# Optimization experiments

Measured on AMD Instinct MI355X. Metric: run time of the kernel, lower is better.

Reference implementation:

```python
import jax, jax.numpy as jnp
import numpy as np
from jax import lax
import math

B, CH, BINS, CROP = 8, 2, 1024, 1024
NUM_BANDS = 4
FF = 2048
EPS = 1e-5
SCALE = 0.02  # weight init scale for numeric stability


def _inorm(x, g, b):
    # InstanceNorm2d: x [B, C, H, W], normalize over (H, W) per (B, C); biased var
    m = x.mean(axis=(2, 3), keepdims=True)
    v = x.var(axis=(2, 3), keepdims=True)
    return (x - m) / jnp.sqrt(v + EPS) * g[None, :, None, None] + b[None, :, None, None]


def _dwconv(x, k):
    # depthwise conv1d: x [B, bins, W], k [bins, 1, 3], padding=1, groups=bins
    return lax.conv_general_dilated(x, k, (1,), [(1, 1)],
                                    dimension_numbers=('NCH', 'OIH', 'NCH'),
                                    feature_group_count=x.shape[1])


def setup_inputs() -> dict:
    key = jax.random.key(0)
    ks = jax.random.split(key, 12)
    inp = {
        'x': jax.random.normal(ks[0], (B, CH, BINS, CROP), jnp.float32),
        'prev_qk': jax.random.normal(ks[1], (B, NUM_BANDS, CROP, CROP), jnp.float32),
        'g_in': jnp.ones((CROP,), jnp.float32),
        'b_in': jnp.zeros((CROP,), jnp.float32),
        'W_in': jax.random.normal(ks[2], (1, CH), jnp.float32) * SCALE,
        'bias_in': jnp.zeros((1,), jnp.float32),
        'g1': jnp.ones((CROP,), jnp.float32),
        'b1': jnp.zeros((CROP,), jnp.float32),
        'Wq': jax.random.normal(ks[3], (BINS, BINS), jnp.float32) * SCALE,
        'Wk': jax.random.normal(ks[4], (BINS, BINS), jnp.float32) * SCALE,
        'Wv': jax.random.normal(ks[5], (BINS, BINS), jnp.float32) * SCALE,
        'Wo': jax.random.normal(ks[6], (BINS, BINS), jnp.float32) * SCALE,
        'kq': jax.random.normal(ks[7], (BINS, 1, 3), jnp.float32) * SCALE,
        'kk': jax.random.normal(ks[8], (BINS, 1, 3), jnp.float32) * SCALE,
        'kv': jax.random.normal(ks[9], (BINS, 1, 3), jnp.float32) * SCALE,
        'pos_w': jax.random.normal(ks[10], (BINS // NUM_BANDS, CROP), jnp.float32) * SCALE,
        'g2': jnp.ones((CROP,), jnp.float32),
        'b2': jnp.zeros((CROP,), jnp.float32),
        'W_ff': jax.random.normal(ks[11], (1, 2), jnp.float32) * SCALE,
        'bias_ff': jnp.zeros((1,), jnp.float32),
        'W1': jax.random.normal(jax.random.fold_in(key, 100), (FF, BINS), jnp.float32) * SCALE,
        'W2': jax.random.normal(jax.random.fold_in(key, 101), (BINS, FF), jnp.float32) * SCALE,
    }
    return inp


def reference(x, prev_qk, g_in, b_in, W_in, bias_in, g1, b1, Wq, Wk, Wv, Wo,
              kq, kk, kv, pos_w, g2, b2, W_ff, bias_ff, W1, W2):
    b = x.shape[0]
    nb = NUM_BANDS
    hd = BINS // nb
    # in_norm + in_project: transposed layout [B, CROP, BINS, CH]
    xt = jnp.transpose(x, (0, 3, 2, 1))
    xt = _inorm(xt, g_in, b_in)
    xt = jnp.einsum('bwhc,oc->bwho', xt, W_in) + bias_in  # [B,CROP,BINS,1]
    x0 = jnp.transpose(xt, (0, 3, 2, 1))                  # [B,1,BINS,CROP]
    # norm1 + attention over frames (w == CROP, c == BINS)
    h = jnp.transpose(_inorm(jnp.transpose(x0, (0, 3, 2, 1)), g1, b1), (0, 3, 2, 1))
    a_in = jnp.transpose(h, (0, 3, 2, 1))[..., 0]         # [B, W, BINS]
    q = jnp.einsum('bwc,oc->bwo', a_in, Wq)
    q = jnp.transpose(_dwconv(jnp.transpose(q, (0, 2, 1)), kq), (0, 2, 1))
    k = jnp.einsum('bwc,oc->bwo', a_in, Wk)
    k = jnp.transpose(_dwconv(jnp.transpose(k, (0, 2, 1)), kk), (0, 2, 1))
    v = jnp.einsum('bwc,oc->bwo', a_in, Wv)
    v = jnp.transpose(_dwconv(jnp.transpose(v, (0, 2, 1)), kv), (0, 2, 1))
    q4 = jnp.transpose(q.reshape(b, CROP, nb, hd), (0, 2, 1, 3))   # [B,nb,W,hd]
    k4 = jnp.transpose(k.reshape(b, CROP, nb, hd), (0, 2, 3, 1))   # [B,nb,hd,W]
    v4 = jnp.transpose(v.reshape(b, CROP, nb, hd), (0, 2, 1, 3))   # [B,nb,W,hd]
    # relative-position bias via pad-and-shift
    p = jnp.matmul(q4, pos_w)                                      # [B,nb,W,CROP]
    p = jnp.pad(p, ((0, 0), (0, 0), (0, 0), (1, 0)))
    p = jnp.swapaxes(p, 2, 3)[:, :, 1:, :]                         # [B,nb,CROP,W]
    qk = (jnp.matmul(q4, k4) + p) / math.sqrt(BINS)
    qk = qk + prev_qk
    a = jax.nn.softmax(qk, axis=-1)
    o = jnp.transpose(jnp.matmul(a, v4), (0, 2, 1, 3)).reshape(b, CROP, BINS)
    o = jnp.einsum('bwc,oc->bwo', o, Wo)                           # [B,W,BINS]
    h4 = jnp.transpose(o[..., None], (0, 3, 2, 1))                 # [B,1,BINS,CROP]
    x1 = jnp.concatenate([x0, h4], axis=1)                         # [B,2,BINS,CROP]
    # norm2 + ff_project + squared-ReLU FFN
    hn = _inorm(jnp.transpose(x1, (0, 3, 2, 1)), g2, b2)           # [B,CROP,BINS,2]
    hn = jnp.einsum('bwhc,oc->bwho', hn, W_ff) + bias_ff           # [B,CROP,BINS,1]
    hn = jnp.transpose(hn, (0, 3, 2, 1))                           # [B,1,BINS,CROP]
    ht = jnp.swapaxes(hn, 2, 3)                                    # [B,1,CROP,BINS]
    ht = jnp.square(jax.nn.relu(jnp.einsum('bowc,fc->bowf', ht, W1)))
    ht = jnp.einsum('bowf,cf->bowc', ht, W2)
    hf = jnp.swapaxes(ht, 2, 3)                                    # [B,1,BINS,CROP]
    out = jnp.concatenate([x1, hf], axis=1)                        # [B,3,BINS,CROP]
    return out, qk
```

## Files before the change

kernel.cpp:

```cpp
#include <hip/hip_runtime.h>
#include <stdint.h>

#define DEVI __device__ __forceinline__

typedef __attribute__((ext_vector_type(8))) short bf16x8;
typedef __attribute__((ext_vector_type(4))) float f32x4;

#define B_    8
#define CROP_ 1024
#define BINS_ 1024
#define NB_   4
#define HD_   256
#define FF_   2048
#define EPSF  1e-5f
#define OUT0_ELEMS (8ull*3ull*1024ull*1024ull)
#define MBYTE (1024ull*1024ull)
#define M1ELEM (1024ll*1024ll)

DEVI unsigned short f2bf(float f) {
  unsigned u = __builtin_bit_cast(unsigned, f);
  u += 0x7fffu + ((u >> 16) & 1u);
  return (unsigned short)(u >> 16);
}
DEVI float bf2f(unsigned short h) {
  unsigned u = ((unsigned)h) << 16;
  return __builtin_bit_cast(float, u);
}

DEVI void gload16(const unsigned short* g, unsigned short* l) {
  __builtin_amdgcn_global_load_lds(
      (const __attribute__((address_space(1))) unsigned int*)g,
      (__attribute__((address_space(3))) unsigned int*)l, 16, 0, 0);
}

DEVI void stage32(const unsigned short* g, unsigned short* lds, int ld, int k0) {
  int t = threadIdx.x;
  int wv = t >> 6, ln = t & 63;
  int srow = wv*32 + (ln >> 2);
  int scol = (ln & 3)*8;
  const unsigned short* gp = g + (size_t)srow*ld + k0 + scol;
  gload16(gp, lds + wv*32*32);
  gload16(gp + (size_t)16*ld, lds + (wv*32 + 16)*32);
}

__global__ __launch_bounds__(256) void k_conv_all(
    const float* __restrict__ Wq, const float* __restrict__ Wk,
    const float* __restrict__ Wv, const float* __restrict__ Wo,
    const float* __restrict__ W1, const float* __restrict__ W2,
    const float* __restrict__ pw,
    unsigned short* __restrict__ WQKVB, unsigned short* __restrict__ WOB,
    unsigned short* __restrict__ W1B, unsigned short* __restrict__ W2B,
    unsigned short* __restrict__ PWT) {
  long long i = (long long)blockIdx.x*256 + threadIdx.x;
  long long stride = (long long)gridDim.x*256;
  const long long total = 8*M1ELEM + (1 << 18);
  for (; i < total; i += stride) {
    if (i < 3*M1ELEM) {
      const float* s = i < M1ELEM ? Wq : (i < 2*M1ELEM ? Wk : Wv);
      WQKVB[i] = f2bf(s[i & (M1ELEM-1)]);
    } else if (i < 4*M1ELEM) { WOB[i-3*M1ELEM] = f2bf(Wo[i-3*M1ELEM]); }
    else if (i < 6*M1ELEM)   { W1B[i-4*M1ELEM] = f2bf(W1[i-4*M1ELEM]); }
    else if (i < 8*M1ELEM)   { W2B[i-6*M1ELEM] = f2bf(W2[i-6*M1ELEM]); }
    else {
      long long j = i - 8*M1ELEM;
      int w = (int)(j >> 8), d = (int)(j & 255);
      PWT[j] = f2bf(pw[d*1024 + w]);
    }
  }
}

__global__ __launch_bounds__(256) void k_instat(const float* __restrict__ x,
                                                float* __restrict__ mean, float* __restrict__ rstd) {
  int b = blockIdx.y, w0 = blockIdx.x*32;
  int t = threadIdx.x, wl = t & 31, p = t >> 5;
  const float* xb = x + (size_t)b*2*BINS_*CROP_ + w0 + wl;
  float s = 0.f, ss = 0.f;
  for (int i = p*256; i < p*256 + 256; ++i) {
    float v = xb[(size_t)i*CROP_];
    s += v; ss += v*v;
  }
  __shared__ float ls[8][32], lss[8][32];
  ls[p][wl] = s; lss[p][wl] = ss;
  __syncthreads();
  if (t < 32) {
    float S = 0.f, SS = 0.f;
    for (int q = 0; q < 8; ++q) { S += ls[q][t]; SS += lss[q][t]; }
    float m = S*(1.f/2048.f);
    float var = SS*(1.f/2048.f) - m*m;
    mean[b*CROP_ + w0 + t] = m;
    rstd[b*CROP_ + w0 + t] = rsqrtf(var + EPSF);
  }
}

__global__ __launch_bounds__(256) void k_x0(const float* __restrict__ x,
    const float* __restrict__ mean, const float* __restrict__ rstd,
    const float* __restrict__ g_in, const float* __restrict__ b_in,
    const float* __restrict__ W_in, const float* __restrict__ bias_in,
    float* __restrict__ outp, float* __restrict__ x0t) {
  int b = blockIdx.z;
  int h0 = blockIdx.y*32, w0 = blockIdx.x*32;
  int tx = threadIdx.x, ty = threadIdx.y;
  float W0 = W_in[0], W1 = W_in[1], bi = bias_in[0];
  float sW = W0 + W1;
  __shared__ float tile[32][33];
  int w = w0 + tx;
  float m = mean[b*CROP_ + w], r = rstd[b*CROP_ + w];
  float coef = r * g_in[w];
  float add = b_in[w]*sW + bi;
  for (int s = 0; s < 4; ++s) {
    int h = h0 + ty + s*8;
    size_t i0 = (((size_t)b*2)*BINS_ + h)*CROP_ + w;
    float v0 = x[i0], v1 = x[i0 + (size_t)BINS_*CROP_];
    float val = coef*(W0*v0 + W1*v1 - m*sW) + add;
    outp[(((size_t)b*3)*BINS_ + h)*CROP_ + w] = val;
    tile[ty + s*8][tx] = val;
  }
  __syncthreads();
  for (int s = 0; s < 4; ++s) {
    int wl = ty + s*8;
    x0t[((size_t)b*CROP_ + w0 + wl)*BINS_ + h0 + tx] = tile[tx][wl];
  }
}

__global__ __launch_bounds__(256) void k_norm1(const float* __restrict__ x0t,
    const float* __restrict__ g1, const float* __restrict__ b1,
    unsigned short* __restrict__ ain) {
  int r = blockIdx.x;
  int w = r & (CROP_ - 1);
  int t = threadIdx.x;
  const float* row = x0t + (size_t)r*BINS_;
  float v[4], s = 0.f, ss = 0.f;
  for (int q = 0; q < 4; ++q) { v[q] = row[t + q*256]; s += v[q]; ss += v[q]*v[q]; }
  for (int off = 32; off; off >>= 1) { s += __shfl_xor(s, off); ss += __shfl_xor(ss, off); }
  __shared__ float red[8];
  int wv = t >> 6;
  if ((t & 63) == 0) { red[wv] = s; red[4 + wv] = ss; }
  __syncthreads();
  s = red[0] + red[1] + red[2] + red[3];
  ss = red[4] + red[5] + red[6] + red[7];
  float m = s*(1.f/1024.f);
  float var = ss*(1.f/1024.f) - m*m;
  float rs = rsqrtf(var + EPSF);
  float g = g1[w], bb = b1[w];
  for (int q = 0; q < 4; ++q)
    ain[(size_t)r*BINS_ + t + q*256] = f2bf((v[q] - m)*rs*g + bb);
}

__global__ __launch_bounds__(256) void k_norm2(const float* __restrict__ x0t,
    const float* __restrict__ o2,
    const float* __restrict__ g2, const float* __restrict__ b2,
    const float* __restrict__ W_ff, const float* __restrict__ bias_ff,
    unsigned short* __restrict__ hn) {
  int r = blockIdx.x;
  int w = r & (CROP_ - 1);
  int t = threadIdx.x;
  const float* ra = x0t + (size_t)r*BINS_;
  const float* rb = o2 + (size_t)r*BINS_;
  float va[4], vb[4], s = 0.f, ss = 0.f;
  for (int q = 0; q < 4; ++q) {
    va[q] = ra[t + q*256]; vb[q] = rb[t + q*256];
    s += va[q] + vb[q]; ss += va[q]*va[q] + vb[q]*vb[q];
  }
  for (int off = 32; off; off >>= 1) { s += __shfl_xor(s, off); ss += __shfl_xor(ss, off); }
  __shared__ float red[8];
  int wv = t >> 6;
  if ((t & 63) == 0) { red[wv] = s; red[4 + wv] = ss; }
  __syncthreads();
  s = red[0] + red[1] + red[2] + red[3];
  ss = red[4] + red[5] + red[6] + red[7];
  float m = s*(1.f/2048.f);
  float var = ss*(1.f/2048.f) - m*m;
  float rs = rsqrtf(var + EPSF);
  float W0 = W_ff[0], W1f = W_ff[1];
  float gg = g2[w]*rs;
  float add = b2[w]*(W0 + W1f) + bias_ff[0];
  for (int q = 0; q < 4; ++q)
    hn[(size_t)r*BINS_ + t + q*256] = f2bf(gg*(W0*(va[q] - m) + W1f*(vb[q] - m)) + add);
}

__global__ __launch_bounds__(256) void k_dwconv(const unsigned short* __restrict__ qkvb,
    const float* __restrict__ kq, const float* __restrict__ kk2, const float* __restrict__ kv,
    unsigned short* __restrict__ qkvc) {
  int w = blockIdx.x, b = blockIdx.y, which = blockIdx.z;
  int t = threadIdx.x;
  const float* kw = which == 0 ? kq : (which == 1 ? kk2 : kv);
  const unsigned short* r0 = qkvb + (size_t)which*8*M1ELEM + ((size_t)b*CROP_ + w)*BINS_;
  unsigned short* d0 = qkvc + (size_t)which*8*M1ELEM + ((size_t)b*CROP_ + w)*BINS_;
  for (int q = 0; q < 4; ++q) {
    int c = t + q*256;
    float k0 = kw[c*3], k1 = kw[c*3 + 1], k2 = kw[c*3 + 2];
    float acc = bf2f(r0[c]) * k1;
    if (w > 0)        acc += bf2f(r0[c - BINS_]) * k0;
    if (w < CROP_-1)  acc += bf2f(r0[c + BINS_]) * k2;
    d0[c] = f2bf(acc);
  }
}

__global__ __launch_bounds__(256) void k_tr_bf16(const unsigned short* __restrict__ src,
                                                 unsigned short* __restrict__ dst) {
  int b = blockIdx.z;
  int w0 = blockIdx.x*32, c0 = blockIdx.y*32;
  int tx = threadIdx.x, ty = threadIdx.y;
  __shared__ unsigned short tile[32][33];
  const unsigned short* S = src + (size_t)b*BINS_*CROP_;
  unsigned short* D = dst + (size_t)b*BINS_*CROP_;
  for (int s = 0; s < 4; ++s)
    tile[ty + s*8][tx] = S[(size_t)(w0 + ty + s*8)*BINS_ + c0 + tx];
  __syncthreads();
  for (int s = 0; s < 4; ++s)
    D[(size_t)(c0 + ty + s*8)*CROP_ + w0 + tx] = tile[tx][ty + s*8];
}

__global__ __launch_bounds__(256) void k_tr_f32_out(const float* __restrict__ src,
                                                    float* __restrict__ outp, int ch) {
  int b = blockIdx.z;
  int w0 = blockIdx.x*32, h0 = blockIdx.y*32;
  int tx = threadIdx.x, ty = threadIdx.y;
  __shared__ float tile[32][33];
  const float* S = src + (size_t)b*CROP_*BINS_;
  for (int s = 0; s < 4; ++s)
    tile[ty + s*8][tx] = S[(size_t)(w0 + ty + s*8)*BINS_ + h0 + tx];
  __syncthreads();
  float* D = outp + (((size_t)b*3 + ch)*BINS_)*CROP_;
  for (int s = 0; s < 4; ++s)
    D[(size_t)(h0 + ty + s*8)*CROP_ + w0 + tx] = tile[tx][ty + s*8];
}

#define BUFB 49152
#define ABYTES 32768

DEVI void stage_ab(const unsigned short* Ab, int lda, const unsigned short* Bb, int ldb,
                   int k0, unsigned short* buf, int t, int wv) {
  int trow = t >> 3;
  int colel = ((t & 7) ^ (trow & 7)) << 3;
  unsigned short* lbase = buf + wv*512;
  const unsigned short* ga = Ab + (size_t)trow*lda + k0 + colel;
#pragma unroll
  for (int c = 0; c < 4; ++c)
    gload16(ga + (size_t)(c*64)*lda, lbase + c*4096);
  const unsigned short* gb = Bb + (size_t)trow*ldb + k0 + colel;
  unsigned short* lbb = buf + 16384 + wv*512;
#pragma unroll
  for (int c = 0; c < 2; ++c)
    gload16(gb + (size_t)(c*64)*ldb, lbb + c*4096);
}

template<int MODE>
__global__ __launch_bounds__(512) void k_gemm3(
    const unsigned short* __restrict__ A, int lda,
    const unsigned short* __restrict__ Bt, int ldb,
    void* __restrict__ C, int ldc, int K)
{
  __shared__ __align__(16) unsigned short lds[3*24576];
  const unsigned short* Ab = A + (size_t)blockIdx.x*256*lda;
  const unsigned short* Bb = Bt + (size_t)blockIdx.y*128*ldb;
  const int t = threadIdx.x;
  const int wv = t >> 6, ln = t & 63;
  const int wm = wv >> 1, wn = wv & 1;
  const int lr = ln & 15, lk = ln >> 4;
  const int sx = (lr & 7) << 4;
  const int NT = K >> 6;
  stage_ab(Ab, lda, Bb, ldb, 0,   lds,           t, wv);
  stage_ab(Ab, lda, Bb, ldb, 64,  lds + 24576,   t, wv);
  stage_ab(Ab, lda, Bb, ldb, 128, lds + 49152,   t, wv);
  asm volatile("s_waitcnt vmcnt(12)" ::: "memory");
  __builtin_amdgcn_s_barrier();

  f32x4 acc[4][4] = {};
  for (int kt = 0; kt < NT; ++kt) {
    const int cur = kt % 3;
    const char* bufc = (const char*)lds + cur*BUFB;
    bf16x8 af[2][4], bf[2][4];
#pragma unroll
    for (int kk = 0; kk < 2; ++kk) {
#pragma unroll
      for (int mi = 0; mi < 4; ++mi) {
        int row = wm*64 + mi*16 + lr;
        af[kk][mi] = *(const bf16x8*)(bufc + ((row*128 + kk*64 + lk*16) ^ sx));
      }
#pragma unroll
      for (int ni = 0; ni < 4; ++ni) {
        int row = wn*64 + ni*16 + lr;
        bf[kk][ni] = *(const bf16x8*)(bufc + ABYTES + ((row*128 + kk*64 + lk*16) ^ sx));
      }
    }
    asm volatile("s_waitcnt lgkmcnt(0)" ::: "memory");
    __builtin_amdgcn_s_barrier();
    if (kt + 3 < NT)
      stage_ab(Ab, lda, Bb, ldb, (kt+3)*64, (unsigned short*)((char*)lds + cur*BUFB), t, wv);
    __builtin_amdgcn_s_setprio(1);
#pragma unroll
    for (int kk = 0; kk < 2; ++kk)
#pragma unroll
      for (int mi = 0; mi < 4; ++mi)
#pragma unroll
        for (int ni = 0; ni < 4; ++ni)
          acc[mi][ni] = __builtin_amdgcn_mfma_f32_16x16x32_bf16(af[kk][mi], bf[kk][ni], acc[mi][ni], 0, 0, 0);
    __builtin_amdgcn_s_setprio(0);
    if (kt + 1 < NT) {
      int rem = (NT-1 < kt+3 ? NT-1 : kt+3) - (kt+1);
      if (rem >= 2)      asm volatile("s_waitcnt vmcnt(12)" ::: "memory");
      else if (rem == 1) asm volatile("s_waitcnt vmcnt(6)"  ::: "memory");
      else               asm volatile("s_waitcnt vmcnt(0)"  ::: "memory");
      __builtin_amdgcn_s_barrier();
    }
  }

  const int row0 = blockIdx.x*256 + wm*64 + lk*4;
  const int col0 = blockIdx.y*128 + wn*64 + lr;
#pragma unroll
  for (int mi = 0; mi < 4; ++mi)
#pragma unroll
    for (int ni = 0; ni < 4; ++ni)
#pragma unroll
      for (int j = 0; j < 4; ++j) {
        int row = row0 + mi*16 + j;
        int col = col0 + ni*16;
        float v = acc[mi][ni][j];
        if (MODE == 0) {
          ((float*)C)[(size_t)row*ldc + col] = v;
        } else if (MODE == 2) {
          float rr = fmaxf(v, 0.f);
          ((unsigned short*)C)[(size_t)row*ldc + col] = f2bf(rr*rr);
        } else {
          ((unsigned short*)C)[(size_t)(col >> 10)*8*M1ELEM + (size_t)row*1024 + (col & 1023)] = f2bf(v);
        }
      }
}

__global__ __launch_bounds__(256) void k_qkpos(
    const unsigned short* __restrict__ qc, const unsigned short* __restrict__ kc,
    const unsigned short* __restrict__ pwt,
    const float* __restrict__ prev, float* __restrict__ qkout,
    float* __restrict__ Mg, float* __restrict__ Lg)
{
  __shared__ __align__(16) unsigned short lA1[128*32], lB1[128*32], lA2[128*32], lB2[128*32];
  const int z = blockIdx.z, b = z >> 2, n = z & 3;
  const size_t bandoff = (size_t)b*CROP_*BINS_ + (size_t)n*HD_;
  const unsigned short* A1 = qc + bandoff + (size_t)blockIdx.x*128*BINS_;
  const unsigned short* B1 = kc + bandoff + (size_t)blockIdx.y*128*BINS_;
  const unsigned short* A2 = pwt + (size_t)blockIdx.x*128*HD_;
  const unsigned short* B2 = qc + bandoff + (size_t)blockIdx.y*128*BINS_;
  const int t = threadIdx.x;
  const int wv = t >> 6, ln = t & 63;
  const int wr = (wv >> 1)*64, wc = (wv & 1)*64;
  const int lr = ln & 15, lk = ln >> 4;
  f32x4 acc[4][4] = {};
  for (int k0 = 0; k0 < HD_; k0 += 32) {
    stage32(A1, lA1, BINS_, k0);
    stage32(B1, lB1, BINS_, k0);
    stage32(A2, lA2, HD_, k0);
    stage32(B2, lB2, BINS_, k0);
    __syncthreads();
    bf16x8 af[4], bfr[4];
#pragma unroll
    for (int mi = 0; mi < 4; ++mi) af[mi]  = *(const bf16x8*)&lA1[(wr + mi*16 + lr)*32 + lk*8];
#pragma unroll
    for (int ni = 0; ni < 4; ++ni) bfr[ni] = *(const bf16x8*)&lB1[(wc + ni*16 + lr)*32 + lk*8];
#pragma unroll
    for (int mi = 0; mi < 4; ++mi)
#pragma unroll
      for (int ni = 0; ni < 4; ++ni)
        acc[mi][ni] = __builtin_amdgcn_mfma_f32_16x16x32_bf16(af[mi], bfr[ni], acc[mi][ni], 0, 0, 0);
#pragma unroll
    for (int mi = 0; mi < 4; ++mi) af[mi]  = *(const bf16x8*)&lA2[(wr + mi*16 + lr)*32 + lk*8];
#pragma unroll
    for (int ni = 0; ni < 4; ++ni) bfr[ni] = *(const bf16x8*)&lB2[(wc + ni*16 + lr)*32 + lk*8];
#pragma unroll
    for (int mi = 0; mi < 4; ++mi)
#pragma unroll
      for (int ni = 0; ni < 4; ++ni)
        acc[mi][ni] = __builtin_amdgcn_mfma_f32_16x16x32_bf16(af[mi], bfr[ni], acc[mi][ni], 0, 0, 0);
    __syncthreads();
  }
  const float* pz = prev + (size_t)z*CROP_*CROP_;
  float* oz = qkout + (size_t)z*CROP_*CROP_;
  const int row0 = blockIdx.x*128 + wr + lk*4;
  const int col0 = blockIdx.y*128 + wc + lr;
  float* smf = (float*)lA1;
  float* slf = smf + 256;
  const int wch = wv & 1;
  const int rbase = wr + lk*4;
#pragma unroll
  for (int mi = 0; mi < 4; ++mi) {
    float v[4][4];
    float tmax[4];
#pragma unroll
    for (int j = 0; j < 4; ++j) tmax[j] = -1e30f;
#pragma unroll
    for (int ni = 0; ni < 4; ++ni)
#pragma unroll
      for (int j = 0; j < 4; ++j) {
        size_t idx = (size_t)(row0 + mi*16 + j)*CROP_ + col0 + ni*16;
        float val = acc[mi][ni][j]*0.03125f + pz[idx];
        oz[idx] = val;
        v[j][ni] = val;
        tmax[j] = fmaxf(tmax[j], val);
      }
#pragma unroll
    for (int off = 1; off < 16; off <<= 1)
#pragma unroll
      for (int j = 0; j < 4; ++j) tmax[j] = fmaxf(tmax[j], __shfl_xor(tmax[j], off));
    if ((ln & 15) == 0)
#pragma unroll
      for (int j = 0; j < 4; ++j) smf[wch*128 + rbase + mi*16 + j] = tmax[j];
    __syncthreads();
    float mrow[4], psum[4];
#pragma unroll
    for (int j = 0; j < 4; ++j) {
      int rl = rbase + mi*16 + j;
      mrow[j] = fmaxf(smf[rl], smf[128 + rl]);
      psum[j] = 0.f;
#pragma unroll
      for (int ni = 0; ni < 4; ++ni) psum[j] += __expf(v[j][ni] - mrow[j]);
    }
#pragma unroll
    for (int off = 1; off < 16; off <<= 1)
#pragma unroll
      for (int j = 0; j < 4; ++j) psum[j] += __shfl_xor(psum[j], off);
    if ((ln & 15) == 0)
#pragma unroll
      for (int j = 0; j < 4; ++j) slf[wch*128 + rbase + mi*16 + j] = psum[j];
    __syncthreads();
    if (wch == 0 && (ln & 15) == 0) {
#pragma unroll
      for (int j = 0; j < 4; ++j) {
        int rl = rbase + mi*16 + j;
        int rg = blockIdx.x*128 + rl;
        size_t si = ((size_t)z*CROP_ + rg)*8 + blockIdx.y;
        Mg[si] = mrow[j];
        Lg[si] = slf[rl] + slf[128 + rl];
      }
    }
  }
}

__global__ __launch_bounds__(256) void k_pv(
    const float* __restrict__ qk, const float* __restrict__ Mg, const float* __restrict__ Lg,
    const unsigned short* __restrict__ vct, unsigned short* __restrict__ ob)
{
  __shared__ __align__(16) unsigned short lA[2*128*32];
  __shared__ __align__(16) unsigned short lB[2*128*32];
  __shared__ float s_m[128], s_il[128];
  const int z = blockIdx.z, b = z >> 2, band = z & 3;
  const int row0 = blockIdx.x*128;
  const int cy = blockIdx.y;
  const float* qkf = qk + (size_t)z*CROP_*CROP_ + (size_t)row0*CROP_;
  const unsigned short* Bb = vct + ((size_t)b*CROP_ + band*HD_ + cy*128)*CROP_;
  const int t = threadIdx.x;
  const int wv = t >> 6, ln = t & 63;
  const int wr = (wv >> 1)*64, wc = (wv & 1)*64;
  const int lr = ln & 15, lk = ln >> 4;
  if (t < 128) {
    size_t rg = (size_t)z*CROP_ + row0 + t;
    float m = -1e30f;
#pragma unroll
    for (int cb = 0; cb < 8; ++cb) m = fmaxf(m, Mg[rg*8 + cb]);
    float l = 0.f;
#pragma unroll
    for (int cb = 0; cb < 8; ++cb) l += Lg[rg*8 + cb]*__expf(Mg[rg*8 + cb] - m);
    s_m[t] = m;
    s_il[t] = 1.f / l;
  }
  __syncthreads();
  f32x4 acc[4][4] = {};
  for (int k0 = 0; k0 < CROP_; k0 += 64) {
#pragma unroll
    for (int chunk = 0; chunk < 2; ++chunk) {
#pragma unroll
      for (int i = 0; i < 4; ++i) {
        int idx = i*256 + t;
        int row = idx >> 3, f4 = idx & 7;
        const float4 vv = *(const float4*)&qkf[(size_t)row*CROP_ + k0 + chunk*32 + f4*4];
        float mr = s_m[row];
        unsigned lo = (unsigned)f2bf(__expf(vv.x - mr)) | ((unsigned)f2bf(__expf(vv.y - mr)) << 16);
        unsigned hi = (unsigned)f2bf(__expf(vv.z - mr)) | ((unsigned)f2bf(__expf(vv.w - mr)) << 16);
        *(uint2*)&lA[chunk*4096 + row*32 + f4*4] = make_uint2(lo, hi);
      }
    }
    stage32(Bb, lB, CROP_, k0);
    stage32(Bb, lB + 4096, CROP_, k0 + 32);
    __syncthreads();
#pragma unroll
    for (int kk = 0; kk < 2; ++kk) {
      bf16x8 af[4], bfr[4];
#pragma unroll
      for (int mi = 0; mi < 4; ++mi) af[mi]  = *(const bf16x8*)&lA[kk*4096 + (wr + mi*16 + lr)*32 + lk*8];
#pragma unroll
      for (int ni = 0; ni < 4; ++ni) bfr[ni] = *(const bf16x8*)&lB[kk*4096 + (wc + ni*16 + lr)*32 + lk*8];
#pragma unroll
      for (int mi = 0; mi < 4; ++mi)
#pragma unroll
        for (int ni = 0; ni < 4; ++ni)
          acc[mi][ni] = __builtin_amdgcn_mfma_f32_16x16x32_bf16(af[mi], bfr[ni], acc[mi][ni], 0, 0, 0);
    }
    __syncthreads();
  }
#pragma unroll
  for (int mi = 0; mi < 4; ++mi)
#pragma unroll
    for (int j = 0; j < 4; ++j) {
      int rl = wr + lk*4 + mi*16 + j;
      float il = s_il[rl];
#pragma unroll
      for (int ni = 0; ni < 4; ++ni) {
        int col = band*HD_ + cy*128 + wc + ni*16 + lr;
        ob[((size_t)b*CROP_ + row0 + rl)*BINS_ + col] = f2bf(acc[mi][ni][j]*il);
      }
    }
}

extern "C" void kernel_launch(void* const* d_in, const int* in_sizes, int n_in,
                              void* d_out, int out_size, void* d_ws, size_t ws_size,
                              hipStream_t stream) {
  (void)in_sizes; (void)n_in; (void)out_size; (void)ws_size;
  const float* x       = (const float*)d_in[0];
  const float* prev_qk = (const float*)d_in[1];
  const float* g_in    = (const float*)d_in[2];
  const float* b_in    = (const float*)d_in[3];
  const float* W_in    = (const float*)d_in[4];
  const float* bias_in = (const float*)d_in[5];
  const float* g1      = (const float*)d_in[6];
  const float* b1      = (const float*)d_in[7];
  const float* Wq      = (const float*)d_in[8];
  const float* Wk      = (const float*)d_in[9];
  const float* Wv      = (const float*)d_in[10];
  const float* Wo      = (const float*)d_in[11];
  const float* kq      = (const float*)d_in[12];
  const float* kk      = (const float*)d_in[13];
  const float* kv      = (const float*)d_in[14];
  const float* pos_w   = (const float*)d_in[15];
  const float* g2      = (const float*)d_in[16];
  const float* b2      = (const float*)d_in[17];
  const float* W_ff    = (const float*)d_in[18];
  const float* bias_ff = (const float*)d_in[19];
  const float* W1      = (const float*)d_in[20];
  const float* W2      = (const float*)d_in[21];

  char* ws = (char*)d_ws;
  unsigned short* WQKVB = (unsigned short*)(ws + 0*MBYTE);
  unsigned short* WOB   = (unsigned short*)(ws + 6*MBYTE);
  unsigned short* W1B   = (unsigned short*)(ws + 8*MBYTE);
  unsigned short* W2B   = (unsigned short*)(ws + 12*MBYTE);
  unsigned short* PWT   = (unsigned short*)(ws + 16*MBYTE);
  float*          SMEAN = (float*)(ws + 16*MBYTE + 512*1024);
  float*          SRSTD = (float*)(ws + 16*MBYTE + 512*1024 + 32*1024);
  float*          Mg    = (float*)(ws + 17*MBYTE);
  float*          Lg    = (float*)(ws + 18*MBYTE);
  float*          X0T   = (float*)(ws + 20*MBYTE);
  unsigned short* AIN   = (unsigned short*)(ws + 52*MBYTE);
  unsigned short* QKVB  = (unsigned short*)(ws + 68*MBYTE);
  unsigned short* QKVC  = (unsigned short*)(ws + 116*MBYTE);
  unsigned short* VCT   = (unsigned short*)(ws + 164*MBYTE);
  unsigned short* OB    = (unsigned short*)(ws + 68*MBYTE);
  float*          O2    = (float*)(ws + 116*MBYTE);
  unsigned short* HN    = (unsigned short*)(ws + 148*MBYTE);
  unsigned short* HT    = (unsigned short*)(ws + 20*MBYTE);
  float*          HT2   = (float*)(ws + 52*MBYTE);

  float* outp  = (float*)d_out;
  float* qkout = outp + OUT0_ELEMS;

  dim3 blk256(256, 1, 1);
  dim3 blk512(512, 1, 1);
  dim3 blk32x8(32, 8, 1);

  k_conv_all<<<8448, blk256, 0, stream>>>(Wq, Wk, Wv, Wo, W1, W2, pos_w,
                                          WQKVB, WOB, W1B, W2B, PWT);
  k_instat<<<dim3(32, 8, 1), blk256, 0, stream>>>(x, SMEAN, SRSTD);
  k_x0<<<dim3(32, 32, 8), blk32x8, 0, stream>>>(x, SMEAN, SRSTD, g_in, b_in, W_in, bias_in, outp, X0T);
  k_norm1<<<8192, blk256, 0, stream>>>(X0T, g1, b1, AIN);
  k_gemm3<5><<<dim3(32, 24, 1), blk512, 0, stream>>>(AIN, 1024, WQKVB, 1024, QKVB, 0, 1024);
  k_dwconv<<<dim3(1024, 8, 3), blk256, 0, stream>>>(QKVB, kq, kk, kv, QKVC);
  k_tr_bf16<<<dim3(32, 32, 8), blk32x8, 0, stream>>>(QKVC + (size_t)2*8*M1ELEM, VCT);
  k_qkpos<<<dim3(8, 8, 32), blk256, 0, stream>>>(QKVC, QKVC + (size_t)8*M1ELEM, PWT,
                                                 prev_qk, qkout, Mg, Lg);
  k_pv<<<dim3(8, 2, 32), blk256, 0, stream>>>(qkout, Mg, Lg, VCT, OB);
  k_gemm3<0><<<dim3(32, 8, 1), blk512, 0, stream>>>(OB, 1024, WOB, 1024, O2, 1024, 1024);
  k_tr_f32_out<<<dim3(32, 32, 8), blk32x8, 0, stream>>>(O2, outp, 1);
  k_norm2<<<8192, blk256, 0, stream>>>(X0T, O2, g2, b2, W_ff, bias_ff, HN);
  k_gemm3<2><<<dim3(32, 16, 1), blk512, 0, stream>>>(HN, 1024, W1B, 1024, HT, 2048, 1024);
  k_gemm3<0><<<dim3(32, 8, 1), blk512, 0, stream>>>(HT, 2048, W2B, 2048, HT2, 1024, 2048);
  k_tr_f32_out<<<dim3(32, 32, 8), blk32x8, 0, stream>>>(HT2, outp, 2);
}
```

Measured before the change: 503.0 us.

## Fuse norm stats with x0, dwconv with V transpose, and retile attention GEMMs

```diff
diff --git a/kernel.cpp b/kernel.cpp
--- a/kernel.cpp
+++ b/kernel.cpp
@@ -31,16 +31,6 @@
   __builtin_amdgcn_global_load_lds(
       (const __attribute__((address_space(1))) unsigned int*)g,
       (__attribute__((address_space(3))) unsigned int*)l, 16, 0, 0);
-}
-
-DEVI void stage32(const unsigned short* g, unsigned short* lds, int ld, int k0) {
-  int t = threadIdx.x;
-  int wv = t >> 6, ln = t & 63;
-  int srow = wv*32 + (ln >> 2);
-  int scol = (ln & 3)*8;
-  const unsigned short* gp = g + (size_t)srow*ld + k0 + scol;
-  gload16(gp, lds + wv*32*32);
-  gload16(gp + (size_t)16*ld, lds + (wv*32 + 16)*32);
 }
 
 __global__ __launch_bounds__(256) void k_conv_all(
@@ -69,56 +59,54 @@
   }
 }
 
-__global__ __launch_bounds__(256) void k_instat(const float* __restrict__ x,
-                                                float* __restrict__ mean, float* __restrict__ rstd) {
+__global__ __launch_bounds__(256) void k_instx0(const float* __restrict__ x,
+    const float* __restrict__ g_in, const float* __restrict__ b_in,
+    const float* __restrict__ W_in, const float* __restrict__ bias_in,
+    float* __restrict__ outp, float* __restrict__ x0t) {
   int b = blockIdx.y, w0 = blockIdx.x*32;
   int t = threadIdx.x, wl = t & 31, p = t >> 5;
-  const float* xb = x + (size_t)b*2*BINS_*CROP_ + w0 + wl;
+  const float* xb = x + (size_t)b*2*M1ELEM + w0 + wl;
   float s = 0.f, ss = 0.f;
   for (int i = p*256; i < p*256 + 256; ++i) {
     float v = xb[(size_t)i*CROP_];
     s += v; ss += v*v;
   }
   __shared__ float ls[8][32], lss[8][32];
+  __shared__ float s_coef[32], s_add[32];
   ls[p][wl] = s; lss[p][wl] = ss;
   __syncthreads();
+  float W0 = W_in[0], W1 = W_in[1], bi = bias_in[0];
+  float sW = W0 + W1;
   if (t < 32) {
     float S = 0.f, SS = 0.f;
     for (int q = 0; q < 8; ++q) { S += ls[q][t]; SS += lss[q][t]; }
     float m = S*(1.f/2048.f);
     float var = SS*(1.f/2048.f) - m*m;
-    mean[b*CROP_ + w0 + t] = m;
-    rstd[b*CROP_ + w0 + t] = rsqrtf(var + EPSF);
-  }
-}
-
-__global__ __launch_bounds__(256) void k_x0(const float* __restrict__ x,
-    const float* __restrict__ mean, const float* __restrict__ rstd,
-    const float* __restrict__ g_in, const float* __restrict__ b_in,
-    const float* __restrict__ W_in, const float* __restrict__ bias_in,
-    float* __restrict__ outp, float* __restrict__ x0t) {
-  int b = blockIdx.z;
-  int h0 = blockIdx.y*32, w0 = blockIdx.x*32;
-  int tx = threadIdx.x, ty = threadIdx.y;
-  float W0 = W_in[0], W1 = W_in[1], bi = bias_in[0];
-  float sW = W0 + W1;
+    float r = rsqrtf(var + EPSF);
+    int w = w0 + t;
+    float coef = r*g_in[w];
+    s_coef[t] = coef;
+    s_add[t] = b_in[w]*sW + bi - coef*m*sW;
+  }
+  __syncthreads();
   __shared__ float tile[32][33];
+  int tx = wl, ty = p;
+  float coef = s_coef[tx], add = s_add[tx];
   int w = w0 + tx;
-  float m = mean[b*CROP_ + w], r = rstd[b*CROP_ + w];
-  float coef = r * g_in[w];
-  float add = b_in[w]*sW + bi;
-  for (int s = 0; s < 4; ++s) {
-    int h = h0 + ty + s*8;
-    size_t i0 = (((size_t)b*2)*BINS_ + h)*CROP_ + w;
-    float v0 = x[i0], v1 = x[i0 + (size_t)BINS_*CROP_];
-    float val = coef*(W0*v0 + W1*v1 - m*sW) + add;
-    outp[(((size_t)b*3)*BINS_ + h)*CROP_ + w] = val;
-    tile[ty + s*8][tx] = val;
-  }
-  __syncthreads();
-  for (int s = 0; s < 4; ++s) {
-    int wl = ty + s*8;
-    x0t[((size_t)b*CROP_ + w0 + wl)*BINS_ + h0 + tx] = tile[tx][wl];
+  for (int h0 = 0; h0 < BINS_; h0 += 32) {
+#pragma unroll
+    for (int q = 0; q < 4; ++q) {
+      int h = h0 + ty + q*8;
+      size_t i0 = ((size_t)b*2*BINS_ + h)*CROP_ + w;
+      float val = coef*(W0*x[i0] + W1*x[i0 + (size_t)M1ELEM]) + add;
+      outp[(((size_t)b*3)*BINS_ + h)*CROP_ + w] = val;
+      tile[ty + q*8][tx] = val;
+    }
+    __syncthreads();
+#pragma unroll
+    for (int q = 0; q < 4; ++q)
+      x0t[((size_t)b*CROP_ + w0 + ty + q*8)*BINS_ + h0 + tx] = tile[tx][ty + q*8];
+    __syncthreads();
   }
 }
 
@@ -179,11 +167,11 @@
 }
 
 __global__ __launch_bounds__(256) void k_dwconv(const unsigned short* __restrict__ qkvb,
-    const float* __restrict__ kq, const float* __restrict__ kk2, const float* __restrict__ kv,
+    const float* __restrict__ kq, const float* __restrict__ kk2,
     unsigned short* __restrict__ qkvc) {
   int w = blockIdx.x, b = blockIdx.y, which = blockIdx.z;
   int t = threadIdx.x;
-  const float* kw = which == 0 ? kq : (which == 1 ? kk2 : kv);
+  const float* kw = which == 0 ? kq : kk2;
   const unsigned short* r0 = qkvb + (size_t)which*8*M1ELEM + ((size_t)b*CROP_ + w)*BINS_;
   unsigned short* d0 = qkvc + (size_t)which*8*M1ELEM + ((size_t)b*CROP_ + w)*BINS_;
   for (int q = 0; q < 4; ++q) {
@@ -196,19 +184,30 @@
   }
 }
 
-__global__ __launch_bounds__(256) void k_tr_bf16(const unsigned short* __restrict__ src,
-                                                 unsigned short* __restrict__ dst) {
+__global__ __launch_bounds__(256) void k_dwconv_trV(const unsigned short* __restrict__ vb,
+    const float* __restrict__ kv, unsigned short* __restrict__ vct) {
   int b = blockIdx.z;
   int w0 = blockIdx.x*32, c0 = blockIdx.y*32;
   int tx = threadIdx.x, ty = threadIdx.y;
-  __shared__ unsigned short tile[32][33];
-  const unsigned short* S = src + (size_t)b*BINS_*CROP_;
-  unsigned short* D = dst + (size_t)b*BINS_*CROP_;
-  for (int s = 0; s < 4; ++s)
-    tile[ty + s*8][tx] = S[(size_t)(w0 + ty + s*8)*BINS_ + c0 + tx];
+  __shared__ unsigned short tile[34][33];
+  const unsigned short* S = vb + (size_t)b*M1ELEM;
+#pragma unroll
+  for (int q = 0; q < 4; ++q) {
+    int wl = ty + q*8;
+    tile[wl + 1][tx] = S[(size_t)(w0 + wl)*BINS_ + c0 + tx];
+  }
+  if (ty == 0) tile[0][tx]  = (w0 > 0)          ? S[(size_t)(w0 - 1)*BINS_ + c0 + tx] : (unsigned short)0;
+  if (ty == 1) tile[33][tx] = (w0 + 32 < CROP_) ? S[(size_t)(w0 + 32)*BINS_ + c0 + tx] : (unsigned short)0;
   __syncthreads();
-  for (int s = 0; s < 4; ++s)
-    D[(size_t)(c0 + ty + s*8)*CROP_ + w0 + tx] = tile[tx][ty + s*8];
+  unsigned short* D = vct + (size_t)b*M1ELEM;
+#pragma unroll
+  for (int q = 0; q < 4; ++q) {
+    int cl = ty + q*8;
+    int c = c0 + cl;
+    float k0 = kv[c*3], k1 = kv[c*3 + 1], k2 = kv[c*3 + 2];
+    float val = k0*bf2f(tile[tx][cl]) + k1*bf2f(tile[tx + 1][cl]) + k2*bf2f(tile[tx + 2][cl]);
+    D[(size_t)c*CROP_ + w0 + tx] = f2bf(val);
+  }
 }
 
 __global__ __launch_bounds__(256) void k_tr_f32_out(const float* __restrict__ src,
@@ -328,59 +327,103 @@
       }
 }
 
-__global__ __launch_bounds__(256) void k_qkpos(
+DEVI void stage_qk(const unsigned short* qc_b, const unsigned short* kc_b,
+                   const unsigned short* pwt, int bx, int by, int k0,
+                   unsigned short* buf, int t, int wv) {
+  int trow = t >> 3;
+  int colel = ((t & 7) ^ (trow & 7)) << 3;
+  unsigned short* lbase = buf + wv*512;
+  if (k0 < 256) {
+    const unsigned short* ga = qc_b + (size_t)(bx*256 + trow)*BINS_ + k0 + colel;
+#pragma unroll
+    for (int c = 0; c < 4; ++c)
+      gload16(ga + (size_t)(c*64)*BINS_, lbase + c*4096);
+  } else {
+    const unsigned short* ga = pwt + (size_t)(bx*256 + trow)*HD_ + (k0 - 256) + colel;
+#pragma unroll
+    for (int c = 0; c < 4; ++c)
+      gload16(ga + (size_t)(c*64)*HD_, lbase + c*4096);
+  }
+  const unsigned short* gbsrc = (k0 < 256) ? kc_b : qc_b;
+  int kb = (k0 < 256) ? k0 : k0 - 256;
+  const unsigned short* gb = gbsrc + (size_t)(by*128 + trow)*BINS_ + kb + colel;
+  unsigned short* lbb = buf + 16384 + wv*512;
+#pragma unroll
+  for (int c = 0; c < 2; ++c)
+    gload16(gb + (size_t)(c*64)*BINS_, lbb + c*4096);
+}
+
+__global__ __launch_bounds__(512) void k_qkpos2(
     const unsigned short* __restrict__ qc, const unsigned short* __restrict__ kc,
     const unsigned short* __restrict__ pwt,
     const float* __restrict__ prev, float* __restrict__ qkout,
     float* __restrict__ Mg, float* __restrict__ Lg)
 {
-  __shared__ __align__(16) unsigned short lA1[128*32], lB1[128*32], lA2[128*32], lB2[128*32];
+  __shared__ __align__(16) unsigned short lds[3*24576];
   const int z = blockIdx.z, b = z >> 2, n = z & 3;
   const size_t bandoff = (size_t)b*CROP_*BINS_ + (size_t)n*HD_;
-  const unsigned short* A1 = qc + bandoff + (size_t)blockIdx.x*128*BINS_;
-  const unsigned short* B1 = kc + bandoff + (size_t)blockIdx.y*128*BINS_;
-  const unsigned short* A2 = pwt + (size_t)blockIdx.x*128*HD_;
-  const unsigned short* B2 = qc + bandoff + (size_t)blockIdx.y*128*BINS_;
+  const unsigned short* qc_b = qc + bandoff;
+  const unsigned short* kc_b = kc + bandoff;
+  const int bx = blockIdx.x, by = blockIdx.y;
   const int t = threadIdx.x;
   const int wv = t >> 6, ln = t & 63;
-  const int wr = (wv >> 1)*64, wc = (wv & 1)*64;
+  const int wm = wv >> 1, wn = wv & 1;
   const int lr = ln & 15, lk = ln >> 4;
+  const int sx = (lr & 7) << 4;
+  const int NT = 8;
+  stage_qk(qc_b, kc_b, pwt, bx, by, 0,   lds,         t, wv);
+  stage_qk(qc_b, kc_b, pwt, bx, by, 64,  lds + 24576, t, wv);
+  stage_qk(qc_b, kc_b, pwt, bx, by, 128, lds + 49152, t, wv);
+  asm volatile("s_waitcnt vmcnt(12)" ::: "memory");
+  __builtin_amdgcn_s_barrier();
+
   f32x4 acc[4][4] = {};
-  for (int k0 = 0; k0 < HD_; k0 += 32) {
-    stage32(A1, lA1, BINS_, k0);
-    stage32(B1, lB1, BINS_, k0);
-    stage32(A2, lA2, HD_, k0);
-    stage32(B2, lB2, BINS_, k0);
-    __syncthreads();
-    bf16x8 af[4], bfr[4];
-#pragma unroll
-    for (int mi = 0; mi < 4; ++mi) af[mi]  = *(const bf16x8*)&lA1[(wr + mi*16 + lr)*32 + lk*8];
-#pragma unroll
-    for (int ni = 0; ni < 4; ++ni) bfr[ni] = *(const bf16x8*)&lB1[(wc + ni*16 + lr)*32 + lk*8];
-#pragma unroll
-    for (int mi = 0; mi < 4; ++mi)
-#pragma unroll
-      for (int ni = 0; ni < 4; ++ni)
-        acc[mi][ni] = __builtin_amdgcn_mfma_f32_16x16x32_bf16(af[mi], bfr[ni], acc[mi][ni], 0, 0, 0);
-#pragma unroll
-    for (int mi = 0; mi < 4; ++mi) af[mi]  = *(const bf16x8*)&lA2[(wr + mi*16 + lr)*32 + lk*8];
-#pragma unroll
-    for (int ni = 0; ni < 4; ++ni) bfr[ni] = *(const bf16x8*)&lB2[(wc + ni*16 + lr)*32 + lk*8];
-#pragma unroll
-    for (int mi = 0; mi < 4; ++mi)
-#pragma unroll
-      for (int ni = 0; ni < 4; ++ni)
-        acc[mi][ni] = __builtin_amdgcn_mfma_f32_16x16x32_bf16(af[mi], bfr[ni], acc[mi][ni], 0, 0, 0);
-    __syncthreads();
-  }
-  const float* pz = prev + (size_t)z*CROP_*CROP_;
-  float* oz = qkout + (size_t)z*CROP_*CROP_;
-  const int row0 = blockIdx.x*128 + wr + lk*4;
-  const int col0 = blockIdx.y*128 + wc + lr;
-  float* smf = (float*)lA1;
-  float* slf = smf + 256;
-  const int wch = wv & 1;
-  const int rbase = wr + lk*4;
+  for (int kt = 0; kt < NT; ++kt) {
+    const int cur = kt % 3;
+    const char* bufc = (const char*)lds + cur*BUFB;
+    bf16x8 af[2][4], bf[2][4];
+#pragma unroll
+    for (int kk = 0; kk < 2; ++kk) {
+#pragma unroll
+      for (int mi = 0; mi < 4; ++mi) {
+        int row = wm*64 + mi*16 + lr;
+        af[kk][mi] = *(const bf16x8*)(bufc + ((row*128 + kk*64 + lk*16) ^ sx));
+      }
+#pragma unroll
+      for (int ni = 0; ni < 4; ++ni) {
+        int row = wn*64 + ni*16 + lr;
+        bf[kk][ni] = *(const bf16x8*)(bufc + ABYTES + ((row*128 + kk*64 + lk*16) ^ sx));
+      }
+    }
+    asm volatile("s_waitcnt lgkmcnt(0)" ::: "memory");
+    __builtin_amdgcn_s_barrier();
+    if (kt + 3 < NT)
+      stage_qk(qc_b, kc_b, pwt, bx, by, (kt+3)*64, (unsigned short*)((char*)lds + cur*BUFB), t, wv);
+    __builtin_amdgcn_s_setprio(1);
+#pragma unroll
+    for (int kk = 0; kk < 2; ++kk)
+#pragma unroll
+      for (int mi = 0; mi < 4; ++mi)
+#pragma unroll
+        for (int ni = 0; ni < 4; ++ni)
+          acc[mi][ni] = __builtin_amdgcn_mfma_f32_16x16x32_bf16(af[kk][mi], bf[kk][ni], acc[mi][ni], 0, 0, 0);
+    __builtin_amdgcn_s_setprio(0);
+    if (kt + 1 < NT) {
+      int rem = (NT-1 < kt+3 ? NT-1 : kt+3) - (kt+1);
+      if (rem >= 2)      asm volatile("s_waitcnt vmcnt(12)" ::: "memory");
+      else if (rem == 1) asm volatile("s_waitcnt vmcnt(6)"  ::: "memory");
+      else               asm volatile("s_waitcnt vmcnt(0)"  ::: "memory");
+      __builtin_amdgcn_s_barrier();
+    }
+  }
+
+  const float* pz = prev + (size_t)z*M1ELEM;
+  float* oz = qkout + (size_t)z*M1ELEM;
+  const int row0g = bx*256;
+  const int col0 = by*128 + wn*64 + lr;
+  float* smf = (float*)lds;
+  float* slf = smf + 512;
+  const int rbase = wm*64 + lk*4;
 #pragma unroll
   for (int mi = 0; mi < 4; ++mi) {
     float v[4][4];
@@ -391,7 +434,7 @@
     for (int ni = 0; ni < 4; ++ni)
 #pragma unroll
       for (int j = 0; j < 4; ++j) {
-        size_t idx = (size_t)(row0 + mi*16 + j)*CROP_ + col0 + ni*16;
+        size_t idx = (size_t)(row0g + rbase + mi*16 + j)*CROP_ + col0 + ni*16;
         float val = acc[mi][ni][j]*0.03125f + pz[idx];
         oz[idx] = val;
         v[j][ni] = val;
@@ -401,15 +444,15 @@
     for (int off = 1; off < 16; off <<= 1)
 #pragma unroll
       for (int j = 0; j < 4; ++j) tmax[j] = fmaxf(tmax[j], __shfl_xor(tmax[j], off));
-    if ((ln & 15) == 0)
-#pragma unroll
-      for (int j = 0; j < 4; ++j) smf[wch*128 + rbase + mi*16 + j] = tmax[j];
+    if (lr == 0)
+#pragma unroll
+      for (int j = 0; j < 4; ++j) smf[wn*256 + rbase + mi*16 + j] = tmax[j];
     __syncthreads();
     float mrow[4], psum[4];
 #pragma unroll
     for (int j = 0; j < 4; ++j) {
       int rl = rbase + mi*16 + j;
-      mrow[j] = fmaxf(smf[rl], smf[128 + rl]);
+      mrow[j] = fmaxf(smf[rl], smf[256 + rl]);
       psum[j] = 0.f;
 #pragma unroll
       for (int ni = 0; ni < 4; ++ni) psum[j] += __expf(v[j][ni] - mrow[j]);
@@ -418,38 +461,37 @@
     for (int off = 1; off < 16; off <<= 1)
 #pragma unroll
       for (int j = 0; j < 4; ++j) psum[j] += __shfl_xor(psum[j], off);
-    if ((ln & 15) == 0)
-#pragma unroll
-      for (int j = 0; j < 4; ++j) slf[wch*128 + rbase + mi*16 + j] = psum[j];
+    if (lr == 0)
+#pragma unroll
+      for (int j = 0; j < 4; ++j) slf[wn*256 + rbase + mi*16 + j] = psum[j];
     __syncthreads();
-    if (wch == 0 && (ln & 15) == 0) {
+    if (wn == 0 && lr == 0) {
 #pragma unroll
       for (int j = 0; j < 4; ++j) {
         int rl = rbase + mi*16 + j;
-        int rg = blockIdx.x*128 + rl;
-        size_t si = ((size_t)z*CROP_ + rg)*8 + blockIdx.y;
+        int rg = row0g + rl;
+        size_t si = ((size_t)z*CROP_ + rg)*8 + by;
         Mg[si] = mrow[j];
-        Lg[si] = slf[rl] + slf[128 + rl];
-      }
-    }
-  }
-}
-
-__global__ __launch_bounds__(256) void k_pv(
+        Lg[si] = slf[rl] + slf[256 + rl];
+      }
+    }
+  }
+}
+
+__global__ __launch_bounds__(512) void k_pv2(
     const float* __restrict__ qk, const float* __restrict__ Mg, const float* __restrict__ Lg,
     const unsigned short* __restrict__ vct, unsigned short* __restrict__ ob)
 {
-  __shared__ __align__(16) unsigned short lA[2*128*32];
-  __shared__ __align__(16) unsigned short lB[2*128*32];
+  __shared__ __align__(16) unsigned short lA[128*64];
+  __shared__ __align__(16) unsigned short lB[256*64];
   __shared__ float s_m[128], s_il[128];
-  const int z = blockIdx.z, b = z >> 2, band = z & 3;
+  const int z = blockIdx.y, b = z >> 2, band = z & 3;
   const int row0 = blockIdx.x*128;
-  const int cy = blockIdx.y;
-  const float* qkf = qk + (size_t)z*CROP_*CROP_ + (size_t)row0*CROP_;
-  const unsigned short* Bb = vct + ((size_t)b*CROP_ + band*HD_ + cy*128)*CROP_;
+  const float* qkf = qk + (size_t)z*M1ELEM + (size_t)row0*CROP_;
+  const unsigned short* Bb = vct + ((size_t)b*CROP_ + band*HD_)*CROP_;
   const int t = threadIdx.x;
   const int wv = t >> 6, ln = t & 63;
-  const int wr = (wv >> 1)*64, wc = (wv & 1)*64;
+  const int wm = wv >> 2, wn = wv & 3;
   const int lr = ln & 15, lk = ln >> 4;
   if (t < 128) {
     size_t rg = (size_t)z*CROP_ + row0 + t;
@@ -463,31 +505,44 @@
     s_il[t] = 1.f / l;
   }
   __syncthreads();
+  const int trow = t >> 3;
+  const int colel = ((t & 7) ^ (trow & 7)) << 3;
   f32x4 acc[4][4] = {};
   for (int k0 = 0; k0 < CROP_; k0 += 64) {
-#pragma unroll
-    for (int chunk = 0; chunk < 2; ++chunk) {
-#pragma unroll
-      for (int i = 0; i < 4; ++i) {
-        int idx = i*256 + t;
+    {
+      const unsigned short* gb = Bb + (size_t)trow*CROP_ + k0 + colel;
+      unsigned short* lbb = lB + wv*512;
+#pragma unroll
+      for (int c = 0; c < 4; ++c)
+        gload16(gb + (size_t)(c*64)*CROP_, lbb + c*4096);
+    }
+#pragma unroll
+    for (int chunk = 0; chunk < 2; ++chunk)
+#pragma unroll
+      for (int i = 0; i < 2; ++i) {
+        int idx = i*512 + t;
         int row = idx >> 3, f4 = idx & 7;
         const float4 vv = *(const float4*)&qkf[(size_t)row*CROP_ + k0 + chunk*32 + f4*4];
         float mr = s_m[row];
         unsigned lo = (unsigned)f2bf(__expf(vv.x - mr)) | ((unsigned)f2bf(__expf(vv.y - mr)) << 16);
         unsigned hi = (unsigned)f2bf(__expf(vv.z - mr)) | ((unsigned)f2bf(__expf(vv.w - mr)) << 16);
-        *(uint2*)&lA[chunk*4096 + row*32 + f4*4] = make_uint2(lo, hi);
-      }
-    }
-    stage32(Bb, lB, CROP_, k0);
-    stage32(Bb, lB + 4096, CROP_, k0 + 32);
+        int byteoff = (row*128 + chunk*64 + f4*8) ^ ((row & 7) << 4);
+        *(uint2*)((char*)lA + byteoff) = make_uint2(lo, hi);
+      }
     __syncthreads();
 #pragma unroll
     for (int kk = 0; kk < 2; ++kk) {
       bf16x8 af[4], bfr[4];
 #pragma unroll
-      for (int mi = 0; mi < 4; ++mi) af[mi]  = *(const bf16x8*)&lA[kk*4096 + (wr + mi*16 + lr)*32 + lk*8];
-#pragma unroll
-      for (int ni = 0; ni < 4; ++ni) bfr[ni] = *(const bf16x8*)&lB[kk*4096 + (wc + ni*16 + lr)*32 + lk*8];
+      for (int mi = 0; mi < 4; ++mi) {
+        int row = wm*64 + mi*16 + lr;
+        af[mi] = *(const bf16x8*)((const char*)lA + ((row*128 + kk*64 + lk*16) ^ ((row & 7) << 4)));
+      }
+#pragma unroll
+      for (int ni = 0; ni < 4; ++ni) {
+        int row = wn*64 + ni*16 + lr;
+        bfr[ni] = *(const bf16x8*)((const char*)lB + ((row*128 + kk*64 + lk*16) ^ ((row & 7) << 4)));
+      }
 #pragma unroll
       for (int mi = 0; mi < 4; ++mi)
 #pragma unroll
@@ -500,11 +555,11 @@
   for (int mi = 0; mi < 4; ++mi)
 #pragma unroll
     for (int j = 0; j < 4; ++j) {
-      int rl = wr + lk*4 + mi*16 + j;
+      int rl = wm*64 + mi*16 + lk*4 + j;
       float il = s_il[rl];
 #pragma unroll
       for (int ni = 0; ni < 4; ++ni) {
-        int col = band*HD_ + cy*128 + wc + ni*16 + lr;
+        int col = band*HD_ + wn*64 + ni*16 + lr;
         ob[((size_t)b*CROP_ + row0 + rl)*BINS_ + col] = f2bf(acc[mi][ni][j]*il);
       }
     }
@@ -543,8 +598,6 @@
   unsigned short* W1B   = (unsigned short*)(ws + 8*MBYTE);
   unsigned short* W2B   = (unsigned short*)(ws + 12*MBYTE);
   unsigned short* PWT   = (unsigned short*)(ws + 16*MBYTE);
-  float*          SMEAN = (float*)(ws + 16*MBYTE + 512*1024);
-  float*          SRSTD = (float*)(ws + 16*MBYTE + 512*1024 + 32*1024);
   float*          Mg    = (float*)(ws + 17*MBYTE);
   float*          Lg    = (float*)(ws + 18*MBYTE);
   float*          X0T   = (float*)(ws + 20*MBYTE);
@@ -567,15 +620,14 @@
 
   k_conv_all<<<8448, blk256, 0, stream>>>(Wq, Wk, Wv, Wo, W1, W2, pos_w,
                                           WQKVB, WOB, W1B, W2B, PWT);
-  k_instat<<<dim3(32, 8, 1), blk256, 0, stream>>>(x, SMEAN, SRSTD);
-  k_x0<<<dim3(32, 32, 8), blk32x8, 0, stream>>>(x, SMEAN, SRSTD, g_in, b_in, W_in, bias_in, outp, X0T);
+  k_instx0<<<dim3(32, 8, 1), blk256, 0, stream>>>(x, g_in, b_in, W_in, bias_in, outp, X0T);
   k_norm1<<<8192, blk256, 0, stream>>>(X0T, g1, b1, AIN);
   k_gemm3<5><<<dim3(32, 24, 1), blk512, 0, stream>>>(AIN, 1024, WQKVB, 1024, QKVB, 0, 1024);
-  k_dwconv<<<dim3(1024, 8, 3), blk256, 0, stream>>>(QKVB, kq, kk, kv, QKVC);
-  k_tr_bf16<<<dim3(32, 32, 8), blk32x8, 0, stream>>>(QKVC + (size_t)2*8*M1ELEM, VCT);
-  k_qkpos<<<dim3(8, 8, 32), blk256, 0, stream>>>(QKVC, QKVC + (size_t)8*M1ELEM, PWT,
-                                                 prev_qk, qkout, Mg, Lg);
-  k_pv<<<dim3(8, 2, 32), blk256, 0, stream>>>(qkout, Mg, Lg, VCT, OB);
+  k_dwconv<<<dim3(1024, 8, 2), blk256, 0, stream>>>(QKVB, kq, kk, QKVC);
+  k_dwconv_trV<<<dim3(32, 32, 8), blk32x8, 0, stream>>>(QKVB + (size_t)2*8*M1ELEM, kv, VCT);
+  k_qkpos2<<<dim3(4, 8, 32), blk512, 0, stream>>>(QKVC, QKVC + (size_t)8*M1ELEM, PWT,
+                                                  prev_qk, qkout, Mg, Lg);
+  k_pv2<<<dim3(8, 32, 1), blk512, 0, stream>>>(qkout, Mg, Lg, VCT, OB);
   k_gemm3<0><<<dim3(32, 8, 1), blk512, 0, stream>>>(OB, 1024, WOB, 1024, O2, 1024, 1024);
   k_tr_f32_out<<<dim3(32, 32, 8), blk32x8, 0, stream>>>(O2, outp, 1);
   k_norm2<<<8192, blk256, 0, stream>>>(X0T, O2, g2, b2, W_ff, bias_ff, HN);
```

Result: faster. 491.4 us (-2.3%).
